# Kernel optimization log

Measured on AMD Instinct MI355X. Metric: run time of the kernel, lower is better.

The kernel has to match this reference:

```python
import jax, jax.numpy as jnp
import numpy as np

HEAD_K_DIM = 128  # linear_key_head_dim (not derivable from weight shapes alone)
EPS_NORM = 1e-6


def _l2norm(x, eps=1e-6):
    return x * jax.lax.rsqrt(jnp.sum(x * x, axis=-1, keepdims=True) + eps)


def setup_inputs() -> dict:
    key = jax.random.key(0)
    ks = jax.random.split(key, 9)
    B, S, H = 2, 1024, 2048
    Hv, Hk, Dk, Dv, K = 32, 16, 128, 128, 4
    key_dim, value_dim = Hk * Dk, Hv * Dv
    C = 2 * key_dim + value_dim  # conv_dim = 8192
    s = 0.02
    return {
        "hidden_states": jax.random.normal(ks[0], (B, S, H), jnp.float32),
        "conv_state": jnp.zeros((B, C, K - 1), jnp.float32),
        "recurrent_state": jnp.zeros((B, Hv, Dk, Dv), jnp.float32),
        "W_qkv": (jax.random.normal(ks[1], (C, H)) * s).astype(jnp.float32),
        "W_z": (jax.random.normal(ks[2], (value_dim, H)) * s).astype(jnp.float32),
        "W_b": (jax.random.normal(ks[3], (Hv, H)) * s).astype(jnp.float32),
        "W_a": (jax.random.normal(ks[4], (Hv, H)) * s).astype(jnp.float32),
        "conv_w": (jax.random.normal(ks[5], (C, K)) * s).astype(jnp.float32),
        "dt_bias": jnp.ones((Hv,), jnp.float32),
        "A_log": jnp.log(jax.random.uniform(ks[6], (Hv,), jnp.float32, 1e-3, 16.0)),
        "norm_weight": jnp.ones((Dv,), jnp.float32),
        "W_out": (jax.random.normal(ks[7], (H, value_dim)) * s).astype(jnp.float32),
    }


def reference(hidden_states, conv_state, recurrent_state, W_qkv, W_z, W_b, W_a,
              conv_w, dt_bias, A_log, norm_weight, W_out):
    B, S, H = hidden_states.shape
    Hv = dt_bias.shape[0]
    Dv = norm_weight.shape[0]
    C, K = conv_w.shape
    value_dim = Hv * Dv
    key_dim = (C - value_dim) // 2
    Dk = HEAD_K_DIM
    Hk = key_dim // Dk

    # input projections
    mixed_qkv = jnp.einsum('bsh,ch->bcs', hidden_states, W_qkv)  # (B, C, S)
    z = hidden_states @ W_z.T                                    # (B, S, value_dim)
    b = hidden_states @ W_b.T                                    # (B, S, Hv)
    a = hidden_states @ W_a.T                                    # (B, S, Hv)

    # causal depthwise conv over time with cached prefix state
    padded = jnp.concatenate([conv_state, mixed_qkv], axis=-1)   # (B, C, K-1+S)
    conv_out = sum(padded[:, :, k:k + S] * conv_w[:, k][None, :, None]
                   for k in range(K))                            # (B, C, S)
    conv_state_new = padded[:, :, -(K - 1):]
    mixed = jnp.swapaxes(jax.nn.silu(conv_out), 1, 2)            # (B, S, C)

    q = mixed[..., :key_dim].reshape(B, S, Hk, Dk)
    k = mixed[..., key_dim:2 * key_dim].reshape(B, S, Hk, Dk)
    v = mixed[..., 2 * key_dim:].reshape(B, S, Hv, Dv)

    beta = jax.nn.sigmoid(b)                                     # (B, S, Hv)
    g = -jnp.exp(A_log) * jax.nn.softplus(a + dt_bias)           # (B, S, Hv)

    rep = Hv // Hk
    if rep > 1:
        q = jnp.repeat(q, rep, axis=2)
        k = jnp.repeat(k, rep, axis=2)

    scale = Dk ** (-0.5)
    q = _l2norm(q) * scale
    k = _l2norm(k)

    # time-leading for scan: (S, B, Hv, ...)
    qT, kT, vT = (jnp.moveaxis(x, 1, 0) for x in (q, k, v))
    gT, betaT = jnp.moveaxis(g, 1, 0), jnp.moveaxis(beta, 1, 0)

    def step(state, xs):
        q_t, k_t, v_t, g_t, beta_t = xs
        state = state * jnp.exp(g_t)[..., None, None]            # decay
        kv_mem = jnp.einsum('bhk,bhkv->bhv', k_t, state)         # read
        delta = (v_t - kv_mem) * beta_t[..., None]               # correction
        state = state + jnp.einsum('bhk,bhv->bhkv', k_t, delta)  # write
        out_t = jnp.einsum('bhk,bhkv->bhv', q_t, state)          # readout
        return state, out_t

    final_state, outs = jax.lax.scan(step, recurrent_state.astype(jnp.float32),
                                     (qT, kT, vT, gT, betaT))
    core = jnp.moveaxis(outs, 0, 1)                              # (B, S, Hv, Dv)

    # gated RMS norm per value head
    var = jnp.mean(core * core, axis=-1, keepdims=True)
    xn = core * jax.lax.rsqrt(var + EPS_NORM) * norm_weight
    gated = xn * jax.nn.silu(z.reshape(B, S, Hv, Dv))

    output = gated.reshape(B, S, value_dim) @ W_out.T            # (B, S, H)
    return output, conv_state_new, final_state
```

## Files before the change

### kernel.cpp

```cpp
#include <hip/hip_runtime.h>
#include <cstdint>
#include <cstddef>

#define B_ 2
#define S_ 1024
#define H_ 2048
#define HV_ 32
#define HK_ 16
#define DK_ 128
#define DV_ 128
#define CC_ 8192
#define KEYDIM_ 2048
#define VALDIM_ 4096
#define NC_ 16
#define CS_ 64
#define NBIG 12416
#define NBIGP 12544

typedef __attribute__((ext_vector_type(8))) short bf16x8;
typedef __attribute__((ext_vector_type(4))) float f32x4;

__device__ __forceinline__ ushort f2bf_rne(float x) {
  union { float f; uint32_t u; } c; c.f = x;
  uint32_t u = c.u + 0x7FFFu + ((c.u >> 16) & 1u);
  return (ushort)(u >> 16);
}

__device__ __forceinline__ void gld16(const void* g, void* l) {
  __builtin_amdgcn_global_load_lds(
      (const __attribute__((address_space(1))) void*)g,
      (__attribute__((address_space(3))) void*)l, 16, 0, 0);
}

__global__ void f2bf_kernel(const float* __restrict__ in, ushort* __restrict__ out, int n) {
  int i = (blockIdx.x * 256 + threadIdx.x) * 4;
  if (i >= n) return;
  float4 v = *(const float4*)(in + i);
  ushort4 o;
  o.x = f2bf_rne(v.x); o.y = f2bf_rne(v.y);
  o.z = f2bf_rne(v.z); o.w = f2bf_rne(v.w);
  *(ushort4*)(out + i) = o;
}

__global__ void wcat_kernel(const float* __restrict__ Wqkv, const float* __restrict__ Wz,
                            const float* __restrict__ Wb, const float* __restrict__ Wa,
                            ushort* __restrict__ out) {
  int i = (blockIdx.x * 256 + threadIdx.x) * 4;
  if (i >= NBIGP * H_) return;
  int n = i >> 11;
  int k = i & (H_ - 1);
  float4 v = make_float4(0.f, 0.f, 0.f, 0.f);
  if (n < 8192)       v = *(const float4*)(Wqkv + (size_t)n * H_ + k);
  else if (n < 12288) v = *(const float4*)(Wz + (size_t)(n - 8192) * H_ + k);
  else if (n < 12320) v = *(const float4*)(Wb + (size_t)(n - 12288) * H_ + k);
  else if (n < 12352) v = *(const float4*)(Wa + (size_t)(n - 12320) * H_ + k);
  ushort4 o;
  o.x = f2bf_rne(v.x); o.y = f2bf_rne(v.y);
  o.z = f2bf_rne(v.z); o.w = f2bf_rne(v.w);
  *(ushort4*)(out + i) = o;
}

#define MEMF() asm volatile("" ::: "memory")
#define VMW(n) asm volatile("s_waitcnt vmcnt(" #n ")" ::: "memory")
#define BARR() do { __builtin_amdgcn_s_barrier(); MEMF(); } while (0)

#define ST(P, SHM, RG, o, kq) do {                                  \
    gld16((P) + (kq),      &SHM[o][((RG) * 2 + 0) * 512]);          \
    gld16((P) + (kq) + 32, &SHM[o][((RG) * 2 + 1) * 512]);          \
  } while (0)

#define LDA(ah, c) do { _Pragma("unroll")                                            \
    for (int i_ = 0; i_ < 4; i_++) { _Pragma("unroll")                               \
      for (int h_ = 0; h_ < 2; h_++)                                                 \
        aF[i_ * 2 + h_] = *(const bf16x8*)(                                          \
            &sAm[c][((wm * 8 + (ah) * 4 + i_) * 2 + h_) * 512 + lane * 8]); } } while (0)

#define LDB(dst, bh, c) do { _Pragma("unroll")                                       \
    for (int j_ = 0; j_ < 2; j_++) { _Pragma("unroll")                               \
      for (int h_ = 0; h_ < 2; h_++)                                                 \
        dst[j_ * 2 + h_] = *(const bf16x8*)(                                         \
            &sBm[c][((wn * 4 + (bh) * 2 + j_) * 2 + h_) * 512 + lane * 8]); } } while (0)

#define MM(ah, bh, bsrc) do {                                                        \
    __builtin_amdgcn_s_setprio(1);                                                   \
    _Pragma("unroll") for (int h_ = 0; h_ < 2; h_++)                                 \
    _Pragma("unroll") for (int i_ = 0; i_ < 4; i_++)                                 \
    _Pragma("unroll") for (int j_ = 0; j_ < 2; j_++)                                 \
      acc[(ah) * 4 + i_][(bh) * 2 + j_] = __builtin_amdgcn_mfma_f32_16x16x32_bf16(   \
          aF[i_ * 2 + h_], bsrc[j_ * 2 + h_], acc[(ah) * 4 + i_][(bh) * 2 + j_],     \
          0, 0, 0);                                                                  \
    __builtin_amdgcn_s_setprio(0);                                                   \
  } while (0)

__global__ __launch_bounds__(512, 2) void gemm256_8ph(
    const ushort* __restrict__ A, const ushort* __restrict__ B,
    float* __restrict__ C, int Ns, int K)
{
  __shared__ ushort sAm[2][16384];
  __shared__ ushort sBm[2][16384];

  const int t = threadIdx.x;
  const int wave = t >> 6, lane = t & 63;
  const int wm = wave >> 2, wn = wave & 3;
  const int l15 = lane & 15, l4 = lane >> 4;
  const int mt = blockIdx.x, nt = blockIdx.y;

  const int rgS0 = (wave & 3) + (wave >> 2) * 8;
  const int rgS3 = rgS0 + 4;
  const int rgS1 = (wave & 1) + (wave >> 1) * 4;
  const int rgS2 = rgS1 + 2;

  const ushort* aP0 = A + (size_t)(mt * 256 + rgS0 * 16 + l15) * K + l4 * 8;
  const ushort* aP1 = A + (size_t)(mt * 256 + rgS3 * 16 + l15) * K + l4 * 8;
  const ushort* bP0 = B + (size_t)(nt * 256 + rgS1 * 16 + l15) * K + l4 * 8;
  const ushort* bP1 = B + (size_t)(nt * 256 + rgS2 * 16 + l15) * K + l4 * 8;

  f32x4 acc[8][4];
  #pragma unroll
  for (int i = 0; i < 8; i++)
    #pragma unroll
    for (int j = 0; j < 4; j++)
      #pragma unroll
      for (int r = 0; r < 4; r++) acc[i][j][r] = 0.f;

  bf16x8 aF[8], bF0[4], bF1[4];

  ST(aP0, sAm, rgS0, 0, 0); MEMF();
  ST(bP0, sBm, rgS1, 0, 0); MEMF();
  ST(bP1, sBm, rgS2, 0, 0); MEMF();
  ST(aP1, sAm, rgS3, 0, 0); MEMF();
  ST(aP0, sAm, rgS0, 1, 64); MEMF();
  VMW(6); BARR();

  const int NT = K >> 6;
  for (int tt = 0; tt < NT; tt++) {
    const int c = tt & 1, o = c ^ 1;
    const int kq1 = (tt + 1 < NT) ? (tt + 1) << 6 : 0;
    const int kq2 = (tt + 2 < NT) ? (tt + 2) << 6 : 0;
    LDA(0, c); LDB(bF0, 0, c);
    VMW(4); BARR();
    ST(bP0, sBm, rgS1, o, kq1); MEMF();
    MM(0, 0, bF0);
    BARR();
    LDB(bF1, 1, c);
    VMW(4); BARR();
    ST(bP1, sBm, rgS2, o, kq1); MEMF();
    MM(0, 1, bF1);
    BARR();
    LDA(1, c);
    VMW(4); BARR();
    ST(aP1, sAm, rgS3, o, kq1); MEMF();
    MM(1, 1, bF1);
    BARR();
    VMW(4); BARR();
    ST(aP0, sAm, rgS0, c, kq2); MEMF();
    MM(1, 0, bF0);
    BARR();
  }
  VMW(0);

  #pragma unroll
  for (int mf = 0; mf < 8; mf++) {
    const int row0 = mt * 256 + wm * 128 + mf * 16 + l4 * 4;
    #pragma unroll
    for (int nf = 0; nf < 4; nf++) {
      const int col = nt * 256 + wn * 64 + nf * 16 + l15;
      if (col < Ns) {
        #pragma unroll
        for (int r = 0; r < 4; r++)
          C[(size_t)(row0 + r) * Ns + col] = acc[mf][nf][r];
      }
    }
  }
}

__device__ __forceinline__ void stage_tile(
    const ushort* aS0, const ushort* aS1, const ushort* bS0, const ushort* bS1,
    ushort* ldsA, ushort* ldsB, int wave, int k0)
{
  #pragma unroll
  for (int h = 0; h < 2; h++) {
    gld16(aS0 + k0 + h * 32, ldsA + h * 4096 + (wave * 2 + 0) * 512);
    gld16(aS1 + k0 + h * 32, ldsA + h * 4096 + (wave * 2 + 1) * 512);
    gld16(bS0 + k0 + h * 32, ldsB + h * 4096 + (wave * 2 + 0) * 512);
    gld16(bS1 + k0 + h * 32, ldsB + h * 4096 + (wave * 2 + 1) * 512);
  }
}

__global__ __launch_bounds__(256) void gemm_bf16_nt(
    const ushort* __restrict__ A, const ushort* __restrict__ B,
    float* __restrict__ C, int M, int N, int K)
{
  __shared__ ushort sL[2][2][8192];
  int t = threadIdx.x;
  int wave = t >> 6, lane = t & 63;
  int wm = wave >> 1, wn = wave & 1;
  int lrow = lane & 15, quad = lane >> 4;
  int mt = blockIdx.x, nt = blockIdx.y;

  f32x4 acc[4][4];
  #pragma unroll
  for (int i = 0; i < 4; i++)
    #pragma unroll
    for (int j = 0; j < 4; j++)
      #pragma unroll
      for (int r = 0; r < 4; r++) acc[i][j][r] = 0.f;

  const ushort* aS0 = A + (size_t)(mt * 128 + (wave * 2 + 0) * 16 + lrow) * K + quad * 8;
  const ushort* aS1 = A + (size_t)(mt * 128 + (wave * 2 + 1) * 16 + lrow) * K + quad * 8;
  const ushort* bS0 = B + (size_t)(nt * 128 + (wave * 2 + 0) * 16 + lrow) * K + quad * 8;
  const ushort* bS1 = B + (size_t)(nt * 128 + (wave * 2 + 1) * 16 + lrow) * K + quad * 8;

  stage_tile(aS0, aS1, bS0, bS1, &sL[0][0][0], &sL[0][1][0], wave, 0);
  __syncthreads();

  const int NK = K >> 6;
  for (int it = 0; it < NK; it++) {
    if (it + 1 < NK)
      stage_tile(aS0, aS1, bS0, bS1,
                 &sL[(it + 1) & 1][0][0], &sL[(it + 1) & 1][1][0],
                 wave, (it + 1) * 64);
    const ushort* bufA = &sL[it & 1][0][0];
    const ushort* bufB = &sL[it & 1][1][0];
    #pragma unroll
    for (int h = 0; h < 2; h++) {
      bf16x8 af[4], bfr[4];
      #pragma unroll
      for (int i = 0; i < 4; i++)
        af[i] = *(const bf16x8*)(bufA + h * 4096 + (wm * 4 + i) * 512 + lane * 8);
      #pragma unroll
      for (int j = 0; j < 4; j++)
        bfr[j] = *(const bf16x8*)(bufB + h * 4096 + (wn * 4 + j) * 512 + lane * 8);
      #pragma unroll
      for (int i = 0; i < 4; i++)
        #pragma unroll
        for (int j = 0; j < 4; j++)
          acc[i][j] = __builtin_amdgcn_mfma_f32_16x16x32_bf16(af[i], bfr[j], acc[i][j], 0, 0, 0);
    }
    __syncthreads();
  }

  #pragma unroll
  for (int i = 0; i < 4; i++) {
    int m_base = mt * 128 + wm * 64 + i * 16 + quad * 4;
    #pragma unroll
    for (int j = 0; j < 4; j++) {
      int n = nt * 128 + wn * 64 + j * 16 + lrow;
      #pragma unroll
      for (int rr = 0; rr < 4; rr++)
        C[(size_t)(m_base + rr) * N + n] = acc[i][j][rr];
    }
  }
}

__global__ void convstate_kernel(const float* __restrict__ Cbig,
                                 float* __restrict__ out)
{
  int idx = blockIdx.x * blockDim.x + threadIdx.x;
  if (idx >= B_ * CC_ * 3) return;
  int j = idx % 3;
  int c = (idx / 3) % CC_;
  int b = idx / (3 * CC_);
  out[idx] = Cbig[((size_t)(b * S_ + (S_ - 3 + j))) * NBIG + c];
}

__global__ __launch_bounds__(128) void prep_qkv(
    const float* __restrict__ Cbig, const float* __restrict__ conv_state,
    const float* __restrict__ conv_w,
    float* __restrict__ Qn, float* __restrict__ Kn, float* __restrict__ Vb)
{
  int group = blockIdx.x, s = blockIdx.y, b = blockIdx.z;
  int t = threadIdx.x;
  int c = group * 128 + t;
  float acc = 0.f;
  #pragma unroll
  for (int kk = 0; kk < 4; kk++) {
    int sp = s - 3 + kk;
    float x = (sp < 0) ? conv_state[((size_t)(b * CC_ + c)) * 3 + (3 + sp)]
                       : Cbig[((size_t)(b * S_ + sp)) * NBIG + c];
    acc += conv_w[c * 4 + kk] * x;
  }
  float val = acc / (1.f + __expf(-acc));

  if (group < 32) {
    __shared__ float red2[2];
    float p = val * val;
    #pragma unroll
    for (int off = 32; off > 0; off >>= 1) p += __shfl_xor(p, off);
    if ((t & 63) == 0) red2[t >> 6] = p;
    __syncthreads();
    float r = rsqrtf(red2[0] + red2[1] + 1e-6f);
    if (group < 16) {
      r *= 0.08838834764831845f;
      Qn[(((size_t)(b * HK_ + group)) * S_ + s) * DK_ + t] = val * r;
    } else {
      Kn[(((size_t)(b * HK_ + (group - 16))) * S_ + s) * DK_ + t] = val * r;
    }
  } else {
    Vb[(((size_t)(b * HV_ + (group - 32))) * S_ + s) * DV_ + t] = val;
  }
}

__global__ void prep_gb(const float* __restrict__ Cbig,
                        const float* __restrict__ A_log, const float* __restrict__ dt_bias,
                        float* __restrict__ g_buf, float* __restrict__ beta_buf)
{
  int idx = blockIdx.x * blockDim.x + threadIdx.x;
  if (idx >= B_ * HV_ * S_) return;
  int s = idx & (S_ - 1);
  int hv = (idx >> 10) & 31;
  int b = idx >> 15;
  float bv = Cbig[((size_t)(b * S_ + s)) * NBIG + 12288 + hv];
  float av = Cbig[((size_t)(b * S_ + s)) * NBIG + 12320 + hv];
  float x = av + dt_bias[hv];
  float sp = (x > 20.f) ? x : log1pf(__expf(x));
  g_buf[idx] = -__expf(A_log[hv]) * sp;
  beta_buf[idx] = 1.f / (1.f + __expf(-bv));
}

__device__ __forceinline__ int swf4(int r, int f) { return r * 32 + (f ^ (r & 31)); }
__device__ __forceinline__ int swf1(int r, int k) {
  return r * 128 + 4 * ((k >> 2) ^ (r & 31)) + (k & 3);
}

__global__ __launch_bounds__(256) void cp_kernel(
    const float* __restrict__ Qn, const float* __restrict__ Kn,
    const float* __restrict__ Vb,
    const float* __restrict__ g_buf, const float* __restrict__ beta_buf,
    float* __restrict__ G_buf, float* __restrict__ M_buf,
    float* __restrict__ KcD, float* __restrict__ D0p)
{
  __shared__ float sK[64 * 128];
  __shared__ float sX[32 * 128];
  __shared__ float sT[64 * 64];
  float* sG  = sT;
  float* sBe = sT + 64;
  float* sA  = sX;
  float* tTw = sX;
  float* tTb = sX;
  float4* sK4 = (float4*)sK;
  float4* sX4 = (float4*)sX;

  const int ch = blockIdx.x;
  const int bh = ch / NC_, c = ch % NC_;
  const int b = bh >> 5, hv = bh & 31, hk = hv >> 1;
  const int s0 = c * CS_;
  const int t = threadIdx.x;
  const size_t gOff = (size_t)bh * S_ + s0;

  float Gw0 = 0.f, Bw0 = 0.f;
  if (t < 64) {
    float gi = g_buf[gOff + t];
    Gw0 = gi;
    #pragma unroll
    for (int off = 1; off < 64; off <<= 1) {
      float o = __shfl_up(Gw0, off);
      if (t >= off) Gw0 += o;
    }
    G_buf[gOff + t] = Gw0;
    sG[t] = Gw0;
    Bw0 = beta_buf[gOff + t];
    sBe[t] = Bw0;
  }
  {
    const float4* src = (const float4*)(Kn + ((size_t)(b * HK_ + hk) * S_ + s0) * DK_);
    #pragma unroll
    for (int u = 0; u < 8; u++) {
      int idx = u * 256 + t;
      sK4[swf4(idx >> 5, idx & 31)] = src[idx];
    }
  }
  __syncthreads();

  const float4* qsrc = (const float4*)(Qn + ((size_t)(b * HK_ + hk) * S_ + s0) * DK_);
  {
    int ti2 = t >> 4, tj = t & 15;
    for (int h = 0; h < 2; h++) {
      #pragma unroll
      for (int u = 0; u < 4; u++) {
        int idx = u * 256 + t;
        sX4[swf4(idx >> 5, idx & 31)] = qsrc[h * 1024 + idx];
      }
      __syncthreads();
      float accM[2][4];
      #pragma unroll
      for (int a = 0; a < 2; a++)
        #pragma unroll
        for (int e = 0; e < 4; e++) accM[a][e] = 0.f;
      for (int k4 = 0; k4 < 32; k4++) {
        float4 qv[2], kv[4];
        qv[0] = sX4[swf4(ti2, k4)];
        qv[1] = sX4[swf4(ti2 + 16, k4)];
        #pragma unroll
        for (int e = 0; e < 4; e++) kv[e] = sK4[swf4(tj + 16 * e, k4)];
        #pragma unroll
        for (int a = 0; a < 2; a++)
          #pragma unroll
          for (int e = 0; e < 4; e++)
            accM[a][e] += qv[a].x * kv[e].x + qv[a].y * kv[e].y +
                          qv[a].z * kv[e].z + qv[a].w * kv[e].w;
      }
      #pragma unroll
      for (int a = 0; a < 2; a++) {
        int iG = h * 32 + ti2 + 16 * a;
        float Gi = sG[iG];
        #pragma unroll
        for (int e = 0; e < 4; e++) {
          int j = tj + 16 * e;
          float m = (j <= iG) ? __expf(Gi - sG[j]) * accM[a][e] : 0.f;
          M_buf[(size_t)ch * 4096 + iG * 64 + j] = m;
        }
      }
      __syncthreads();
    }
  }

  {
    int ti = t >> 4, tj = t & 15;
    float accA[4][4];
    #pragma unroll
    for (int a = 0; a < 4; a++)
      #pragma unroll
      for (int e = 0; e < 4; e++) accA[a][e] = 0.f;
    for (int k4 = 0; k4 < 32; k4++) {
      float4 ki[4], kj[4];
      #pragma unroll
      for (int e = 0; e < 4; e++) {
        ki[e] = sK4[swf4(ti + 16 * e, k4)];
        kj[e] = sK4[swf4(tj + 16 * e, k4)];
      }
      #pragma unroll
      for (int a = 0; a < 4; a++)
        #pragma unroll
        for (int e = 0; e < 4; e++)
          accA[a][e] += ki[a].x * kj[e].x + ki[a].y * kj[e].y +
                        ki[a].z * kj[e].z + ki[a].w * kj[e].w;
    }
    float resA[4][4];
    #pragma unroll
    for (int a = 0; a < 4; a++) {
      int i = ti + 16 * a;
      float Gi = sG[i], Bi = sBe[i];
      #pragma unroll
      for (int e = 0; e < 4; e++) {
        int j = tj + 16 * e;
        resA[a][e] = (j < i) ? Bi * __expf(Gi - sG[j]) * accA[a][e] : 0.f;
      }
    }
    __syncthreads();
    #pragma unroll
    for (int a = 0; a < 4; a++)
      #pragma unroll
      for (int e = 0; e < 4; e++)
        sA[(ti + 16 * a) * 64 + (tj + 16 * e)] = resA[a][e];
  }
  __syncthreads();

  if (t < 64) {
    sT[t] = (t == 0) ? 1.f : 0.f;
    for (int i = 1; i < 64; i++) {
      float acc = 0.f;
      for (int j = 0; j < i; j++) acc += sA[i * 64 + j] * sT[j * 64 + t];
      sT[i * 64 + t] = ((t == i) ? 1.f : 0.f) - acc;
    }
    float w = Bw0 * __expf(Gw0);
    for (int j = 0; j < 64; j++) {
      float wj = __shfl(w, j);
      tTw[j * 64 + t] = sT[t * 64 + j] * wj;
    }
  }
  __syncthreads();

  {
    int i04 = t >> 4, tk = t & 15;
    float accK[4][8];
    #pragma unroll
    for (int r = 0; r < 4; r++)
      #pragma unroll
      for (int u = 0; u < 8; u++) accK[r][u] = 0.f;
    for (int j = 0; j < 64; j++) {
      float4 tw = ((float4*)tTw)[j * 16 + i04];
      #pragma unroll
      for (int u = 0; u < 8; u++) {
        float kv = sK[swf1(j, tk + 16 * u)];
        accK[0][u] += tw.x * kv; accK[1][u] += tw.y * kv;
        accK[2][u] += tw.z * kv; accK[3][u] += tw.w * kv;
      }
    }
    size_t base = (size_t)ch * NBIG;
    #pragma unroll
    for (int r = 0; r < 4; r++)
      #pragma unroll
      for (int u = 0; u < 8; u++)
        KcD[base + (i04 * 4 + r) * 128 + tk + 16 * u] = accK[r][u];
  }
  __syncthreads();

  if (t < 64) {
    for (int j = 0; j < 64; j++) {
      float bj = __shfl(Bw0, j);
      tTb[j * 64 + t] = sT[t * 64 + j] * bj;
    }
  }
  {
    const float4* src = (const float4*)(Vb + ((size_t)bh * S_ + s0) * DV_);
    #pragma unroll
    for (int u = 0; u < 8; u++) {
      int idx = u * 256 + t;
      sK4[swf4(idx >> 5, idx & 31)] = src[idx];
    }
  }
  __syncthreads();

  {
    int i04 = t >> 4, tv_ = t & 15;
    float accD[4][8];
    #pragma unroll
    for (int r = 0; r < 4; r++)
      #pragma unroll
      for (int u = 0; u < 8; u++) accD[r][u] = 0.f;
    for (int j = 0; j < 64; j++) {
      float4 tb = ((float4*)tTb)[j * 16 + i04];
      #pragma unroll
      for (int u = 0; u < 8; u++) {
        float vv = sK[swf1(j, tv_ + 16 * u)];
        accD[0][u] += tb.x * vv; accD[1][u] += tb.y * vv;
        accD[2][u] += tb.z * vv; accD[3][u] += tb.w * vv;
      }
    }
    size_t base = (size_t)ch * NBIG;
    #pragma unroll
    for (int r = 0; r < 4; r++)
      #pragma unroll
      for (int u = 0; u < 8; u++)
        D0p[base + (i04 * 4 + r) * 128 + tv_ + 16 * u] = accD[r][u];
  }
}

__global__ __launch_bounds__(512) void phaseb_kernel(
    const float* __restrict__ rec_state, const float* __restrict__ Qn,
    const float* __restrict__ Kn, const float* __restrict__ G_buf,
    float* __restrict__ KcD, const float* __restrict__ D0p,
    float* __restrict__ Oq_buf, float* __restrict__ final_state)
{
  __shared__ float sS[128 * 32];
  __shared__ float sKT[128 * 64];
  __shared__ float sQT[128 * 64];
  __shared__ float sD[64 * 32];
  __shared__ float sR[2][64 * 32];

  const int blk = blockIdx.x;
  const int bh = (blk & 7) | ((blk >> 5) << 3);
  const int vq = (blk >> 3) & 3;
  const int b = bh >> 5, hv = bh & 31, hk = hv >> 1;
  const int t = threadIdx.x;
  const int vbase = vq * 32;
  const float* gG = G_buf + (size_t)bh * S_;

  #pragma unroll
  for (int u = 0; u < 2; u++) {
    int idx = u * 512 + t;
    int k = idx >> 3;
    int v4 = (idx & 7) * 4;
    *(float4*)(&sS[k * 32 + v4]) =
        *(const float4*)(&rec_state[((size_t)bh * 128 + k) * 128 + vbase + v4]);
  }
  __syncthreads();

  const int si = t & 63, skq = t >> 6;
  const int kg = t >> 8;
  const int tt = t & 255;
  const int ti = tt >> 3, tv = t & 7;
  const int tp = t >> 3;

  for (int c = 0; c < NC_; c++) {
    const size_t ch = (size_t)bh * NC_ + c;
    const int s0 = c * CS_;
    const float GC = gG[s0 + 63];
    const float eGC = __expf(GC);

    {
      float eGi = __expf(gG[s0 + si]);
      const float* kcRow = KcD + ch * NBIG + si * 128 + skq * 16;
      const float* qRow  = Qn + ((size_t)(b * HK_ + hk) * S_ + s0 + si) * DK_ + skq * 16;
      #pragma unroll
      for (int u = 0; u < 4; u++) {
        float4 kc = *(const float4*)(kcRow + u * 4);
        float4 qv = *(const float4*)(qRow + u * 4);
        int kk = skq * 16 + u * 4;
        sKT[(kk + 0) * 64 + si] = kc.x; sKT[(kk + 1) * 64 + si] = kc.y;
        sKT[(kk + 2) * 64 + si] = kc.z; sKT[(kk + 3) * 64 + si] = kc.w;
        sQT[(kk + 0) * 64 + si] = qv.x * eGi; sQT[(kk + 1) * 64 + si] = qv.y * eGi;
        sQT[(kk + 2) * 64 + si] = qv.z * eGi; sQT[(kk + 3) * 64 + si] = qv.w * eGi;
      }
    }
    __syncthreads();

    {
      float accD[2][4], accO[2][4];
      #pragma unroll
      for (int r = 0; r < 2; r++) {
        accO[r][0] = accO[r][1] = accO[r][2] = accO[r][3] = 0.f;
        accD[r][0] = accD[r][1] = accD[r][2] = accD[r][3] = 0.f;
      }
      if (kg == 0) {
        #pragma unroll
        for (int r = 0; r < 2; r++) {
          float4 d0 = *(const float4*)(&D0p[ch * NBIG + (size_t)(ti * 2 + r) * 128 + vbase + tv * 4]);
          accD[r][0] = d0.x; accD[r][1] = d0.y; accD[r][2] = d0.z; accD[r][3] = d0.w;
        }
      }
      const int k0 = kg << 6;
      for (int k = k0; k < k0 + 64; k++) {
        float2 kc = *(const float2*)(&sKT[k * 64 + ti * 2]);
        float2 qb = *(const float2*)(&sQT[k * 64 + ti * 2]);
        float4 sv = *(const float4*)(&sS[k * 32 + tv * 4]);
        accD[0][0] -= kc.x * sv.x; accD[0][1] -= kc.x * sv.y;
        accD[0][2] -= kc.x * sv.z; accD[0][3] -= kc.x * sv.w;
        accD[1][0] -= kc.y * sv.x; accD[1][1] -= kc.y * sv.y;
        accD[1][2] -= kc.y * sv.z; accD[1][3] -= kc.y * sv.w;
        accO[0][0] += qb.x * sv.x; accO[0][1] += qb.x * sv.y;
        accO[0][2] += qb.x * sv.z; accO[0][3] += qb.x * sv.w;
        accO[1][0] += qb.y * sv.x; accO[1][1] += qb.y * sv.y;
        accO[1][2] += qb.y * sv.z; accO[1][3] += qb.y * sv.w;
      }
      if (kg == 1) {
        #pragma unroll
        for (int r = 0; r < 2; r++) {
          int i = ti * 2 + r;
          *(float4*)(&sR[0][i * 32 + tv * 4]) =
              make_float4(accD[r][0], accD[r][1], accD[r][2], accD[r][3]);
          *(float4*)(&sR[1][i * 32 + tv * 4]) =
              make_float4(accO[r][0], accO[r][1], accO[r][2], accO[r][3]);
        }
      }
      __syncthreads();
      if (kg == 0) {
        #pragma unroll
        for (int r = 0; r < 2; r++) {
          int i = ti * 2 + r;
          float4 pD = *(const float4*)(&sR[0][i * 32 + tv * 4]);
          float4 pO = *(const float4*)(&sR[1][i * 32 + tv * 4]);
          float4 dv = make_float4(accD[r][0] + pD.x, accD[r][1] + pD.y,
                                  accD[r][2] + pD.z, accD[r][3] + pD.w);
          float4 ov = make_float4(accO[r][0] + pO.x, accO[r][1] + pO.y,
                                  accO[r][2] + pO.z, accO[r][3] + pO.w);
          *(float4*)(&sD[i * 32 + tv * 4]) = dv;
          *(float4*)(&KcD[ch * NBIG + (size_t)i * 128 + vbase + tv * 4]) = dv;
          *(float4*)(&Oq_buf[ch * 8192 + (size_t)i * 128 + vbase + tv * 4]) = ov;
        }
      }
    }

    {
      float sc = __expf(GC - gG[s0 + si]);
      const float* kRow = Kn + ((size_t)(b * HK_ + hk) * S_ + s0 + si) * DK_ + skq * 16;
      #pragma unroll
      for (int u = 0; u < 4; u++) {
        float4 x = *(const float4*)(kRow + u * 4);
        x.x *= sc; x.y *= sc; x.z *= sc; x.w *= sc;
        int kgr = skq * 4 + u;
        *(float4*)(&sKT[si * 128 + 4 * (kgr ^ (si & 31))]) = x;
      }
    }
    __syncthreads();

    {
      float acc[2][4];
      acc[0][0] = acc[0][1] = acc[0][2] = acc[0][3] = 0.f;
      acc[1][0] = acc[1][1] = acc[1][2] = acc[1][3] = 0.f;
      const int kgr = tp >> 1, kh = (tp & 1) * 2;
      for (int i = 0; i < 64; i++) {
        float4 d  = *(const float4*)(&sD[i * 32 + tv * 4]);
        float2 ka = *(const float2*)(&sKT[i * 128 + 4 * (kgr ^ (i & 31)) + kh]);
        acc[0][0] += ka.x * d.x; acc[0][1] += ka.x * d.y;
        acc[0][2] += ka.x * d.z; acc[0][3] += ka.x * d.w;
        acc[1][0] += ka.y * d.x; acc[1][1] += ka.y * d.y;
        acc[1][2] += ka.y * d.z; acc[1][3] += ka.y * d.w;
      }
      #pragma unroll
      for (int r = 0; r < 2; r++) {
        int k = tp * 2 + r;
        float4 s = *(const float4*)(&sS[k * 32 + tv * 4]);
        s.x = s.x * eGC + acc[r][0]; s.y = s.y * eGC + acc[r][1];
        s.z = s.z * eGC + acc[r][2]; s.w = s.w * eGC + acc[r][3];
        *(float4*)(&sS[k * 32 + tv * 4]) = s;
      }
    }
    __syncthreads();
  }

  #pragma unroll
  for (int u = 0; u < 2; u++) {
    int idx = u * 512 + t;
    int k = idx >> 3;
    int v4 = (idx & 7) * 4;
    *(float4*)(&final_state[((size_t)bh * 128 + k) * 128 + vbase + v4]) =
        *(const float4*)(&sS[k * 32 + v4]);
  }
}

__global__ __launch_bounds__(128) void phasec_kernel(
    const float* __restrict__ KcD, const float* __restrict__ Oq_buf,
    const float* __restrict__ M_buf, const float* __restrict__ norm_weight,
    const float* __restrict__ Cbig, ushort* __restrict__ zg_bf)
{
  __shared__ float sM[4096];
  __shared__ float red[2][2];
  int ch = blockIdx.x;
  int bh = ch / NC_, c = ch % NC_;
  int b = bh >> 5, hv = bh & 31;
  int s0 = c * CS_;
  int v = threadIdx.x;

  float Dr[64];
  #pragma unroll
  for (int j = 0; j < 64; j++) Dr[j] = KcD[(size_t)ch * NBIG + j * 128 + v];
  {
    const float4* src = (const float4*)(M_buf + (size_t)ch * 4096);
    #pragma unroll
    for (int u = 0; u < 8; u++) ((float4*)sM)[u * 128 + v] = src[u * 128 + v];
  }
  __syncthreads();
  float nw = norm_weight[v];

  for (int i = 0; i < 64; i++) {
    float o = Oq_buf[(size_t)ch * 8192 + i * 128 + v];
    const float4* mr = (const float4*)(sM + i * 64);
    #pragma unroll
    for (int j4 = 0; j4 < 16; j4++) {
      float4 m = mr[j4];
      o += m.x * Dr[4 * j4] + m.y * Dr[4 * j4 + 1] +
           m.z * Dr[4 * j4 + 2] + m.w * Dr[4 * j4 + 3];
    }
    float p = o * o;
    #pragma unroll
    for (int off = 32; off > 0; off >>= 1) p += __shfl_xor(p, off);
    if ((v & 63) == 0) red[i & 1][v >> 6] = p;
    __syncthreads();
    float var = (red[i & 1][0] + red[i & 1][1]) * (1.f / 128.f);
    float xn = o * rsqrtf(var + 1e-6f) * nw;
    float zv = Cbig[((size_t)(b * S_ + s0 + i)) * NBIG + 8192 + hv * DV_ + v];
    zg_bf[((size_t)(b * S_ + s0 + i)) * VALDIM_ + hv * DV_ + v] =
        f2bf_rne(xn * (zv / (1.f + __expf(-zv))));
  }
}

extern "C" void kernel_launch(void* const* d_in, const int* in_sizes, int n_in,
                              void* d_out, int out_size, void* d_ws, size_t ws_size,
                              hipStream_t stream)
{
  const float* hs          = (const float*)d_in[0];
  const float* conv_state  = (const float*)d_in[1];
  const float* rec_state   = (const float*)d_in[2];
  const float* W_qkv       = (const float*)d_in[3];
  const float* W_z         = (const float*)d_in[4];
  const float* W_b         = (const float*)d_in[5];
  const float* W_a         = (const float*)d_in[6];
  const float* conv_w      = (const float*)d_in[7];
  const float* dt_bias     = (const float*)d_in[8];
  const float* A_log       = (const float*)d_in[9];
  const float* norm_weight = (const float*)d_in[10];
  const float* W_out       = (const float*)d_in[11];

  float* out       = (float*)d_out;
  float* out_conv  = out + (size_t)B_ * S_ * H_;
  float* out_state = out_conv + (size_t)B_ * CC_ * 3;

  float* ws = (float*)d_ws;
  float* Cbig = ws;
  float* KcD  = Cbig;
  float* D0p  = Cbig + (size_t)1024 * NBIG;
  float* g_buf    = ws + 25427968;
  float* beta_buf = ws + 25493504;
  float* G_buf    = ws + 25559040;
  float* Qn       = ws + 25624576;
  float* Kn       = ws + 29818880;
  float* Vb       = ws + 34013184;
  float* M_buf    = ws + 42401792;
  float* Oq_buf   = Vb;

  ushort* Wcat_bf = (ushort*)(ws + 25427968);
  ushort* hs_bf   = (ushort*)(ws + 38273024);
  ushort* zg_bf   = (ushort*)Qn;
  ushort* Wout_bf = (ushort*)Kn;

  const int M = B_ * S_;

  f2bf_kernel<<<(M * H_) / 1024, 256, 0, stream>>>(hs, hs_bf, M * H_);
  wcat_kernel<<<(NBIGP * H_) / 1024, 256, 0, stream>>>(W_qkv, W_z, W_b, W_a, Wcat_bf);
  gemm256_8ph<<<dim3(M / 256, NBIGP / 256), 512, 0, stream>>>(hs_bf, Wcat_bf, Cbig, NBIG, H_);
  convstate_kernel<<<(B_ * CC_ * 3 + 255) / 256, 256, 0, stream>>>(Cbig, out_conv);
  prep_qkv<<<dim3(64, S_, B_), 128, 0, stream>>>(Cbig, conv_state, conv_w, Qn, Kn, Vb);
  prep_gb<<<(B_ * HV_ * S_ + 255) / 256, 256, 0, stream>>>(Cbig, A_log, dt_bias, g_buf, beta_buf);
  cp_kernel<<<B_ * HV_ * NC_, 256, 0, stream>>>(Qn, Kn, Vb, g_buf, beta_buf,
                                                G_buf, M_buf, KcD, D0p);
  phaseb_kernel<<<B_ * HV_ * 4, 512, 0, stream>>>(rec_state, Qn, Kn, G_buf,
                                                  KcD, D0p, Oq_buf, out_state);
  f2bf_kernel<<<(H_ * VALDIM_) / 1024, 256, 0, stream>>>(W_out, Wout_bf, H_ * VALDIM_);
  phasec_kernel<<<B_ * HV_ * NC_, 128, 0, stream>>>(KcD, Oq_buf, M_buf,
                                                    norm_weight, Cbig, zg_bf);
  gemm_bf16_nt<<<dim3(M / 128, H_ / 128), 256, 0, stream>>>(zg_bf, Wout_bf, out, M, H_, VALDIM_);
}
```

Measured before the change: 916.7 us.

## Restructure GEMM main loop into two half-K phases with simpler prefetch schedule

Replaces the 8-phase ping-pong schedule of the 256x256 bf16 GEMM with a two-phase-per-tile loop. Each phase loads all A and B fragments for one 32-wide K half, issues the global-to-LDS prefetch for the next tile, then runs 32 MFMAs. This halves the number of barriers per K tile and drops the two-tile-ahead prefetch. The trade-off is higher register pressure from holding 8 A and 4 B fragments at once, and possibly less overlap of LDS reads with MFMAs.

```diff
diff --git a/kernel.cpp b/kernel.cpp
--- a/kernel.cpp
+++ b/kernel.cpp
@@ -62,35 +62,8 @@
 
 #define MEMF() asm volatile("" ::: "memory")
 #define VMW(n) asm volatile("s_waitcnt vmcnt(" #n ")" ::: "memory")
+#define LGKM(n) asm volatile("s_waitcnt lgkmcnt(" #n ")" ::: "memory")
 #define BARR() do { __builtin_amdgcn_s_barrier(); MEMF(); } while (0)
-
-#define ST(P, SHM, RG, o, kq) do {                                  \
-    gld16((P) + (kq),      &SHM[o][((RG) * 2 + 0) * 512]);          \
-    gld16((P) + (kq) + 32, &SHM[o][((RG) * 2 + 1) * 512]);          \
-  } while (0)
-
-#define LDA(ah, c) do { _Pragma("unroll")                                            \
-    for (int i_ = 0; i_ < 4; i_++) { _Pragma("unroll")                               \
-      for (int h_ = 0; h_ < 2; h_++)                                                 \
-        aF[i_ * 2 + h_] = *(const bf16x8*)(                                          \
-            &sAm[c][((wm * 8 + (ah) * 4 + i_) * 2 + h_) * 512 + lane * 8]); } } while (0)
-
-#define LDB(dst, bh, c) do { _Pragma("unroll")                                       \
-    for (int j_ = 0; j_ < 2; j_++) { _Pragma("unroll")                               \
-      for (int h_ = 0; h_ < 2; h_++)                                                 \
-        dst[j_ * 2 + h_] = *(const bf16x8*)(                                         \
-            &sBm[c][((wn * 4 + (bh) * 2 + j_) * 2 + h_) * 512 + lane * 8]); } } while (0)
-
-#define MM(ah, bh, bsrc) do {                                                        \
-    __builtin_amdgcn_s_setprio(1);                                                   \
-    _Pragma("unroll") for (int h_ = 0; h_ < 2; h_++)                                 \
-    _Pragma("unroll") for (int i_ = 0; i_ < 4; i_++)                                 \
-    _Pragma("unroll") for (int j_ = 0; j_ < 2; j_++)                                 \
-      acc[(ah) * 4 + i_][(bh) * 2 + j_] = __builtin_amdgcn_mfma_f32_16x16x32_bf16(   \
-          aF[i_ * 2 + h_], bsrc[j_ * 2 + h_], acc[(ah) * 4 + i_][(bh) * 2 + j_],     \
-          0, 0, 0);                                                                  \
-    __builtin_amdgcn_s_setprio(0);                                                   \
-  } while (0)
 
 __global__ __launch_bounds__(512, 2) void gemm256_8ph(
     const ushort* __restrict__ A, const ushort* __restrict__ B,
@@ -123,39 +96,52 @@
       #pragma unroll
       for (int r = 0; r < 4; r++) acc[i][j][r] = 0.f;
 
-  bf16x8 aF[8], bF0[4], bF1[4];
-
-  ST(aP0, sAm, rgS0, 0, 0); MEMF();
-  ST(bP0, sBm, rgS1, 0, 0); MEMF();
-  ST(bP1, sBm, rgS2, 0, 0); MEMF();
-  ST(aP1, sAm, rgS3, 0, 0); MEMF();
-  ST(aP0, sAm, rgS0, 1, 64); MEMF();
-  VMW(6); BARR();
+  bf16x8 aF[8], bF[4];
+
+  gld16(aP0,      &sAm[0][(rgS0 * 2 + 0) * 512]);
+  gld16(aP1,      &sAm[0][(rgS3 * 2 + 0) * 512]);
+  gld16(bP0,      &sBm[0][(rgS1 * 2 + 0) * 512]);
+  gld16(bP1,      &sBm[0][(rgS2 * 2 + 0) * 512]);
+  MEMF();
+  gld16(aP0 + 32, &sAm[0][(rgS0 * 2 + 1) * 512]);
+  gld16(aP1 + 32, &sAm[0][(rgS3 * 2 + 1) * 512]);
+  gld16(bP0 + 32, &sBm[0][(rgS1 * 2 + 1) * 512]);
+  gld16(bP1 + 32, &sBm[0][(rgS2 * 2 + 1) * 512]);
+  MEMF();
+  VMW(4); BARR();
 
   const int NT = K >> 6;
   for (int tt = 0; tt < NT; tt++) {
     const int c = tt & 1, o = c ^ 1;
-    const int kq1 = (tt + 1 < NT) ? (tt + 1) << 6 : 0;
-    const int kq2 = (tt + 2 < NT) ? (tt + 2) << 6 : 0;
-    LDA(0, c); LDB(bF0, 0, c);
-    VMW(4); BARR();
-    ST(bP0, sBm, rgS1, o, kq1); MEMF();
-    MM(0, 0, bF0);
-    BARR();
-    LDB(bF1, 1, c);
-    VMW(4); BARR();
-    ST(bP1, sBm, rgS2, o, kq1); MEMF();
-    MM(0, 1, bF1);
-    BARR();
-    LDA(1, c);
-    VMW(4); BARR();
-    ST(aP1, sAm, rgS3, o, kq1); MEMF();
-    MM(1, 1, bF1);
-    BARR();
-    VMW(4); BARR();
-    ST(aP0, sAm, rgS0, c, kq2); MEMF();
-    MM(1, 0, bF0);
-    BARR();
+    const int kq = (tt + 1 < NT) ? (tt + 1) << 6 : 0;
+    #pragma unroll
+    for (int h = 0; h < 2; h++) {
+      #pragma unroll
+      for (int i = 0; i < 8; i++)
+        aF[i] = *(const bf16x8*)(&sAm[c][((wm * 8 + i) * 2 + h) * 512 + lane * 8]);
+      #pragma unroll
+      for (int j = 0; j < 4; j++)
+        bF[j] = *(const bf16x8*)(&sBm[c][((wn * 4 + j) * 2 + h) * 512 + lane * 8]);
+      MEMF();
+      gld16(aP0 + kq + h * 32, &sAm[o][(rgS0 * 2 + h) * 512]);
+      gld16(aP1 + kq + h * 32, &sAm[o][(rgS3 * 2 + h) * 512]);
+      gld16(bP0 + kq + h * 32, &sBm[o][(rgS1 * 2 + h) * 512]);
+      gld16(bP1 + kq + h * 32, &sBm[o][(rgS2 * 2 + h) * 512]);
+      MEMF();
+      LGKM(8);
+      BARR();
+      LGKM(0);
+      __builtin_amdgcn_sched_barrier(0);
+      __builtin_amdgcn_s_setprio(1);
+      #pragma unroll
+      for (int i = 0; i < 8; i++)
+        #pragma unroll
+        for (int j = 0; j < 4; j++)
+          acc[i][j] = __builtin_amdgcn_mfma_f32_16x16x32_bf16(aF[i], bF[j], acc[i][j], 0, 0, 0);
+      __builtin_amdgcn_s_setprio(0);
+      VMW(4);
+      BARR();
+    }
   }
   VMW(0);
 
```

Result: faster. 882.7 us (-3.7%).
